# Kernel tuning notes

Hardware: AMD Instinct MI355X
Metric: run time of the kernel (lower is better)

## Reference

```python
import jax, jax.numpy as jnp
import numpy as np

N_P, E_P = 50000, 400000
N_L, E_L = 50000, 400000
B = 256  # number of graphs per side
NEG_GAT = 0.2   # GATv2 leaky-relu slope
NEG_FC = 0.01   # nn.LeakyReLU default slope


def _gatv2(x, ei, Wl, Wr, att, b, H, C):
    """GATv2Conv (concat heads, add_self_loops=True). Wl/Wr: [in, H*C], att: [H, C], b: [H*C]."""
    N = x.shape[0]
    sl = jnp.arange(N)
    src = jnp.concatenate([ei[0], sl])
    dst = jnp.concatenate([ei[1], sl])
    xl = (x @ Wl).reshape(N, H, C)   # source transform (messages)
    xr = (x @ Wr).reshape(N, H, C)   # target transform
    e = jax.nn.leaky_relu(xl[src] + xr[dst], NEG_GAT)          # [E+N, H, C]
    logits = jnp.einsum('ehc,hc->eh', e, att)                   # [E+N, H]
    m = jax.ops.segment_max(logits, dst, num_segments=N)        # segment softmax
    a = jnp.exp(logits - m[dst])
    alpha = a / jax.ops.segment_sum(a, dst, num_segments=N)[dst]
    out = jax.ops.segment_sum(xl[src] * alpha[..., None], dst, num_segments=N)
    return out.reshape(N, H * C) + b


def _mean_pool(x, batch, nb):
    s = jax.ops.segment_sum(x, batch, num_segments=nb)
    c = jax.ops.segment_sum(jnp.ones((x.shape[0],), x.dtype), batch, num_segments=nb)
    return s / jnp.maximum(c, 1.0)[:, None]


def setup_inputs() -> dict:
    key = jax.random.key(0)
    ks = jax.random.split(key, 48)
    i = [0]
    def nrm(shape, fan_in):
        k = ks[i[0]]; i[0] += 1
        return jax.random.normal(k, shape, jnp.float32) / np.sqrt(fan_in)
    inp = {}
    inp['protein_x'] = jax.random.normal(ks[40], (N_P, 10), jnp.float32)
    inp['ligand_x'] = jax.random.normal(ks[41], (N_L, 5), jnp.float32)
    inp['protein_edge_index'] = jax.random.randint(ks[42], (2, E_P), 0, N_P)
    inp['ligand_edge_index'] = jax.random.randint(ks[43], (2, E_L), 0, N_L)
    inp['protein_batch'] = (jnp.arange(N_P) * B) // N_P  # sorted graph ids, all segments nonempty
    inp['ligand_batch'] = (jnp.arange(N_L) * B) // N_L
    # GATv2 params: layer1 heads=2 out=128, layer2 heads=1 out=256
    inp['p1_Wl'] = nrm((10, 256), 10); inp['p1_Wr'] = nrm((10, 256), 10)
    inp['p1_att'] = nrm((2, 128), 128); inp['p1_b'] = jnp.zeros((256,), jnp.float32)
    inp['p2_Wl'] = nrm((256, 256), 256); inp['p2_Wr'] = nrm((256, 256), 256)
    inp['p2_att'] = nrm((1, 256), 256); inp['p2_b'] = jnp.zeros((256,), jnp.float32)
    inp['l1_Wl'] = nrm((5, 256), 5); inp['l1_Wr'] = nrm((5, 256), 5)
    inp['l1_att'] = nrm((2, 128), 128); inp['l1_b'] = jnp.zeros((256,), jnp.float32)
    inp['l2_Wl'] = nrm((256, 256), 256); inp['l2_Wr'] = nrm((256, 256), 256)
    inp['l2_att'] = nrm((1, 256), 256); inp['l2_b'] = jnp.zeros((256,), jnp.float32)
    # MultiheadAttention(256, 4) params ([in, out] convention)
    inp['Wq'] = nrm((256, 256), 256); inp['bq'] = jnp.zeros((256,), jnp.float32)
    inp['Wk'] = nrm((256, 256), 256); inp['bk'] = jnp.zeros((256,), jnp.float32)
    inp['Wv'] = nrm((256, 256), 256); inp['bv'] = jnp.zeros((256,), jnp.float32)
    inp['Wo'] = nrm((256, 256), 256); inp['bo'] = jnp.zeros((256,), jnp.float32)
    # fc head
    inp['fc1_w'] = nrm((512, 256), 512); inp['fc1_b'] = jnp.zeros((256,), jnp.float32)
    inp['ln_g'] = jnp.ones((256,), jnp.float32); inp['ln_b'] = jnp.zeros((256,), jnp.float32)
    inp['fc2_w'] = nrm((256, 1), 256); inp['fc2_b'] = jnp.zeros((1,), jnp.float32)
    return inp


def reference(protein_x, protein_edge_index, protein_batch,
              ligand_x, ligand_edge_index, ligand_batch,
              p1_Wl, p1_Wr, p1_att, p1_b, p2_Wl, p2_Wr, p2_att, p2_b,
              l1_Wl, l1_Wr, l1_att, l1_b, l2_Wl, l2_Wr, l2_att, l2_b,
              Wq, bq, Wk, bk, Wv, bv, Wo, bo,
              fc1_w, fc1_b, ln_g, ln_b, fc2_w, fc2_b):
    px = _gatv2(protein_x, protein_edge_index, p1_Wl, p1_Wr, p1_att, p1_b, 2, 128)
    px = _gatv2(px, protein_edge_index, p2_Wl, p2_Wr, p2_att, p2_b, 1, 256)
    px = _mean_pool(px, protein_batch, B)                        # [B, 256]
    lx = _gatv2(ligand_x, ligand_edge_index, l1_Wl, l1_Wr, l1_att, l1_b, 2, 128)
    lx = _gatv2(lx, ligand_edge_index, l2_Wl, l2_Wr, l2_att, l2_b, 1, 256)
    lx = _mean_pool(lx, ligand_batch, B)                         # [B, 256]
    # cross attention with q/k/v seq length 1
    D, H = 256, 4
    d = D // H
    qh = (px @ Wq + bq).reshape(B, H, d)
    kh = (lx @ Wk + bk).reshape(B, H, d)
    vh = (lx @ Wv + bv).reshape(B, H, d)
    scores = (qh * kh).sum(-1) / jnp.sqrt(jnp.float32(d))        # [B, H], 1 key
    w = jax.nn.softmax(scores[..., None], axis=-1)               # all ones (single key)
    attn = (w * vh).reshape(B, D) @ Wo + bo                      # [B, 256]
    comb = jnp.concatenate([px, attn], axis=1)                   # [B, 512]
    h = comb @ fc1_w + fc1_b
    mu = h.mean(-1, keepdims=True)
    var = h.var(-1, keepdims=True)
    h = (h - mu) / jnp.sqrt(var + 1e-5) * ln_g + ln_b
    h = jax.nn.leaky_relu(h, NEG_FC)
    return h @ fc2_w + fc2_b                                     # [B, 1]
```

## Files before the change

### kernel.cpp

```cpp
#include <hip/hip_runtime.h>
#include <math.h>

typedef unsigned short u16;
typedef __attribute__((ext_vector_type(8))) short bf16x8;
typedef __attribute__((ext_vector_type(4))) float f32x4;

__device__ inline u16 f2bf(float x) {
  unsigned int u = __float_as_uint(x);
  u += 0x7fffu + ((u >> 16) & 1u);
  return (u16)(u >> 16);
}
__device__ inline float bf2f(u16 h) {
  return __uint_as_float(((unsigned int)h) << 16);
}
__device__ inline float4 ld_bf4(const u16* p) {
  ushort4 v = *(const ushort4*)p;
  return make_float4(bf2f(v.x), bf2f(v.y), bf2f(v.z), bf2f(v.w));
}

__global__ void k_setup(int* __restrict__ cnt, int nz,
                        const float* __restrict__ W2pl, const float* __restrict__ W2pr,
                        const float* __restrict__ W2ll, const float* __restrict__ W2lr,
                        u16* __restrict__ Whp, u16* __restrict__ Wlp,
                        u16* __restrict__ Whl, u16* __restrict__ Wll_o,
                        const float* __restrict__ xp, int Kp, int Np,
                        const float* __restrict__ xl_, int Kl, int Nl,
                        const float* __restrict__ W1pl, const float* __restrict__ W1pr,
                        const float* __restrict__ W1ll, const float* __restrict__ W1lr,
                        u16* __restrict__ xlh_p, u16* __restrict__ xrh_p,
                        u16* __restrict__ xlh_l, u16* __restrict__ xrh_l,
                        int linPer) {
  const int zb = (nz + 255) / 256;
  if ((int)blockIdx.x < zb) {
    int i = blockIdx.x * 256 + threadIdx.x;
    if (i < nz) cnt[i] = 0;
    return;
  }
  int wb = blockIdx.x - zb;
  if (wb < 1024) {
    int n = wb & 511;
    int side = wb >> 9;
    int col = n & 255;
    int k = threadIdx.x;
    const float* W = side == 0 ? (n < 256 ? W2pl : W2pr) : (n < 256 ? W2ll : W2lr);
    float w = W[k * 256 + col];
    u16* Wh = side ? Whl : Whp;
    u16* Wlo = side ? Wll_o : Wlp;
    u16 hb = f2bf(w);
    Wh[n * 256 + k] = hb;
    Wlo[n * 256 + k] = f2bf(w - bf2f(hb));
    return;
  }
  int wb2 = wb - 1024;
  const int side = wb2 / linPer;
  const float* x = side ? xl_ : xp;
  const int K = side ? Kl : Kp;
  const int N = side ? Nl : Np;
  const float* Wl = side ? W1ll : W1pl;
  const float* Wr = side ? W1lr : W1pr;
  u16* xlh = side ? xlh_l : xlh_p;
  u16* xrh = side ? xrh_l : xrh_p;
  int base = (wb2 - side * linPer) * 8;
  if (base >= N) return;
  int j = threadIdx.x;
  __shared__ float xs[16][8];
  int tot = 8 * K;
  for (int i = j; i < tot; i += 256) {
    int r = i / K, k = i - r * K;
    if (base + r < N) xs[k][r] = x[(size_t)(base + r) * K + k];
  }
  __syncthreads();
  float al[8] = {}, ar[8] = {};
  for (int k = 0; k < K; ++k) {
    float wl = Wl[k * 256 + j];
    float wr = Wr[k * 256 + j];
#pragma unroll
    for (int r = 0; r < 8; ++r) {
      al[r] = fmaf(xs[k][r], wl, al[r]);
      ar[r] = fmaf(xs[k][r], wr, ar[r]);
    }
  }
#pragma unroll
  for (int r = 0; r < 8; ++r) {
    int n = base + r;
    if (n < N) {
      xlh[(size_t)n * 256 + j] = f2bf(al[r]);
      xrh[(size_t)n * 256 + j] = f2bf(ar[r]);
    }
  }
}

__global__ void k_histb(const int* __restrict__ eip, int Ep, const int* __restrict__ eil,
                        int El, int* __restrict__ cntp, int* __restrict__ cntl) {
  int e = blockIdx.x * blockDim.x + threadIdx.x;
  if (e < Ep) atomicAdd(&cntp[eip[Ep + e]], 1);
  else if (e < Ep + El) { int e2 = e - Ep; atomicAdd(&cntl[eil[El + e2]], 1); }
}

__global__ void k_scan1b(const int* __restrict__ cntp, int Np, const int* __restrict__ cntl,
                         int Nl, int nbp, int* __restrict__ offsp, int* __restrict__ offsl,
                         int* __restrict__ curp, int* __restrict__ curl,
                         int* __restrict__ bsum) {
  __shared__ int s[256];
  int tid = threadIdx.x;
  int side = ((int)blockIdx.x >= nbp) ? 1 : 0;
  int blk = side ? (blockIdx.x - nbp) : blockIdx.x;
  const int* cnt = side ? cntl : cntp;
  int* offs = side ? offsl : offsp;
  int* cur = side ? curl : curp;
  int N = side ? Nl : Np;
  int i = blk * 256 + tid;
  int v = (i < N) ? cnt[i] : 0;
  if (i < N) cur[i] = 0;
  s[tid] = v;
  __syncthreads();
  for (int off = 1; off < 256; off <<= 1) {
    int t = 0;
    if (tid >= off) t = s[tid - off];
    __syncthreads();
    if (tid >= off) s[tid] += t;
    __syncthreads();
  }
  if (i < N) offs[i] = s[tid] - v;
  if (tid == 255) bsum[side * 256 + blk] = s[255];
}

__global__ void k_scan2b(int* __restrict__ bsum, int nbp, int nbl) {
  __shared__ int s[256];
  int side = blockIdx.x;
  int nb = side ? nbl : nbp;
  int* bs = bsum + side * 256;
  int tid = threadIdx.x;
  int v = (tid < nb) ? bs[tid] : 0;
  s[tid] = v;
  __syncthreads();
  for (int off = 1; off < 256; off <<= 1) {
    int t = 0;
    if (tid >= off) t = s[tid - off];
    __syncthreads();
    if (tid >= off) s[tid] += t;
    __syncthreads();
  }
  if (tid < nb) bs[tid] = s[tid] - v;
}

__global__ void k_fillb(const int* __restrict__ eip, int Ep, const int* __restrict__ eil,
                        int El, const int* __restrict__ offsp, const int* __restrict__ offsl,
                        const int* __restrict__ bsum,
                        int* __restrict__ curp, int* __restrict__ curl,
                        int* __restrict__ csrp, int* __restrict__ csrl) {
  int e = blockIdx.x * blockDim.x + threadIdx.x;
  if (e < Ep) {
    int d = eip[Ep + e];
    int pos = offsp[d] + bsum[d >> 8] + atomicAdd(&curp[d], 1);
    csrp[pos] = eip[e];
  } else if (e < Ep + El) {
    int e2 = e - Ep;
    int d = eil[El + e2];
    int pos = offsl[d] + bsum[256 + (d >> 8)] + atomicAdd(&curl[d], 1);
    csrl[pos] = eil[e2];
  }
}

__global__ void __launch_bounds__(256, 2) k_mm_dual_b(
    const u16* __restrict__ A_p, const u16* __restrict__ A_l,
    const u16* __restrict__ Bh_p, const u16* __restrict__ Bl_p,
    const u16* __restrict__ Bh_l, const u16* __restrict__ Bl_l,
    u16* __restrict__ XLh_p, u16* __restrict__ XRh_p,
    u16* __restrict__ XLh_l, u16* __restrict__ XRh_l, int Np, int Nl, int Rp, int Rtot) {
  __shared__ __align__(16) char smem[32768];
  char* sA = smem;
  char* sBh = smem + 8192;
  char* sBl = smem + 16384;
  const int gid = blockIdx.x;
  const int rblk = (gid >> 5) * 8 + (gid & 7);
  const int col = (gid >> 3) & 3;
  if (rblk >= Rtot) return;
  const int side = (rblk >= Rp) ? 1 : 0;
  const int rloc = side ? rblk - Rp : rblk;
  const u16* A = side ? A_l : A_p;
  const u16* Bhi = side ? Bh_l : Bh_p;
  const u16* Blo = side ? Bl_l : Bl_p;
  u16* XLh = side ? XLh_l : XLh_p;
  u16* XRh = side ? XRh_l : XRh_p;
  const int M = side ? Nl : Np;
  const int t = threadIdx.x;
  const int rowBase = rloc * 128;
  const int j0 = col * 128;
  const int srow = t >> 1;
  const int h = t & 1;
  int gr = rowBase + srow;
  if (gr >= M) gr = M - 1;
  const size_t gaBase = (size_t)gr * 256 + h * 16;
  const size_t gbBase = (size_t)(j0 + srow) * 256 + h * 16;
  const int rb = srow * 64;
  const int sw0 = (((h * 2) + (srow >> 1)) & 3) * 16;
  const int sw1 = (((h * 2 + 1) + (srow >> 1)) & 3) * 16;
  const int lane = t & 63;
  const int wid = t >> 6;
  const int wm = (wid & 1) * 64;
  const int wn = (wid >> 1) * 64;
  const int kq = lane >> 4;
  const int mr = lane & 15;
  int offA[4], offB[4];
#pragma unroll
  for (int i = 0; i < 4; ++i) {
    int m = wm + i * 16 + mr;
    offA[i] = m * 64 + ((kq + (m >> 1)) & 3) * 16;
    int n = wn + i * 16 + mr;
    offB[i] = n * 64 + ((kq + (n >> 1)) & 3) * 16;
  }
  f32x4 acc[4][4] = {};
  uint4 va0 = *(const uint4*)(A + gaBase);
  uint4 va1 = *(const uint4*)(A + gaBase + 8);
  uint4 vbh0 = *(const uint4*)(Bhi + gbBase);
  uint4 vbh1 = *(const uint4*)(Bhi + gbBase + 8);
  uint4 vbl0 = *(const uint4*)(Blo + gbBase);
  uint4 vbl1 = *(const uint4*)(Blo + gbBase + 8);
#pragma unroll
  for (int kt = 0; kt < 8; ++kt) {
    __syncthreads();
    *(uint4*)(sA + rb + sw0) = va0;
    *(uint4*)(sA + rb + sw1) = va1;
    *(uint4*)(sBh + rb + sw0) = vbh0;
    *(uint4*)(sBh + rb + sw1) = vbh1;
    *(uint4*)(sBl + rb + sw0) = vbl0;
    *(uint4*)(sBl + rb + sw1) = vbl1;
    __syncthreads();
    if (kt < 7) {
      const int k0 = (kt + 1) * 32;
      va0 = *(const uint4*)(A + gaBase + k0);
      va1 = *(const uint4*)(A + gaBase + k0 + 8);
      vbh0 = *(const uint4*)(Bhi + gbBase + k0);
      vbh1 = *(const uint4*)(Bhi + gbBase + k0 + 8);
      vbl0 = *(const uint4*)(Blo + gbBase + k0);
      vbl1 = *(const uint4*)(Blo + gbBase + k0 + 8);
    }
    bf16x8 a[4], bh[4], bl[4];
#pragma unroll
    for (int i = 0; i < 4; ++i) {
      a[i] = *(const bf16x8*)(sA + offA[i]);
      bh[i] = *(const bf16x8*)(sBh + offB[i]);
      bl[i] = *(const bf16x8*)(sBl + offB[i]);
    }
#pragma unroll
    for (int i = 0; i < 4; ++i)
#pragma unroll
      for (int j = 0; j < 4; ++j) {
        acc[i][j] = __builtin_amdgcn_mfma_f32_16x16x32_bf16(a[i], bh[j], acc[i][j], 0, 0, 0);
        acc[i][j] = __builtin_amdgcn_mfma_f32_16x16x32_bf16(a[i], bl[j], acc[i][j], 0, 0, 0);
      }
  }
  __syncthreads();
  u16* wtile = (u16*)(smem + wid * 8192);
#pragma unroll
  for (int i = 0; i < 4; ++i)
#pragma unroll
    for (int j = 0; j < 4; ++j)
#pragma unroll
      for (int r = 0; r < 4; ++r)
        wtile[(i * 16 + kq * 4 + r) * 64 + j * 16 + mr] = f2bf(acc[i][j][r]);
  u16* cbase = (col < 2) ? XLh : XRh;
  const int cb = (col < 2) ? j0 : j0 - 256;
  const int r8 = lane >> 3;
  const int c8 = lane & 7;
#pragma unroll
  for (int rr = 0; rr < 8; ++rr) {
    int lr = rr * 8 + r8;
    uint4 v = *(const uint4*)&wtile[lr * 64 + c8 * 8];
    int row = rowBase + wm + lr;
    if (row < M) *(uint4*)&cbase[(size_t)row * 256 + cb + wn + c8 * 8] = v;
  }
}

#define GAT_DOT(a, q)                                                          \
  {                                                                            \
    float t0 = a.x + rd.x, t1 = a.y + rd.y, t2 = a.z + rd.z, t3 = a.w + rd.w;  \
    q = fmaf(t3, wa6.w, fabsf(t3) * wa4.w);                                    \
    q = fmaf(fabsf(t2), wa4.z, fmaf(t2, wa6.z, q));                            \
    q = fmaf(fabsf(t1), wa4.y, fmaf(t1, wa6.y, q));                            \
    q = fmaf(fabsf(t0), wa4.x, fmaf(t0, wa6.x, q));                            \
  }

template <int H>
__global__ void k_gat_gather_b(
    const u16* __restrict__ xlh_p, const u16* __restrict__ xrh_p, u16* __restrict__ out_p,
    const u16* __restrict__ xlh_l, const u16* __restrict__ xrh_l, u16* __restrict__ out_l,
    const int* __restrict__ csr_p, const int* __restrict__ offs_p,
    const int* __restrict__ cnt_p,
    const int* __restrict__ csr_l, const int* __restrict__ offs_l,
    const int* __restrict__ cnt_l, const int* __restrict__ bsum,
    const float* __restrict__ att_p, const float* __restrict__ bias_p,
    const float* __restrict__ att_l, const float* __restrict__ bias_l,
    int Np, int Nl) {
  const int side = blockIdx.y;
  const u16* xlh = side ? xlh_l : xlh_p;
  const u16* xrh = side ? xrh_l : xrh_p;
  u16* out = side ? out_l : out_p;
  const int* csr = side ? csr_l : csr_p;
  const int* offs = side ? offs_l : offs_p;
  const int* cnt = side ? cnt_l : cnt_p;
  const float* att = side ? att_l : att_p;
  const float* bias = side ? bias_l : bias_p;
  const int N = side ? Nl : Np;
  int d = blockIdx.x * 4 + (threadIdx.x >> 6);
  if (d >= N) return;
  const int lo4 = (threadIdx.x & 63) * 4;
  const float4 rd = ld_bf4(&xrh[(size_t)d * 256 + lo4]);
  const float4 wa = *(const float4*)&att[lo4];
  const float4 wa6 = make_float4(0.6f * wa.x, 0.6f * wa.y, 0.6f * wa.z, 0.6f * wa.w);
  const float4 wa4 = make_float4(0.4f * wa.x, 0.4f * wa.y, 0.4f * wa.z, 0.4f * wa.w);
  const float4 xd = ld_bf4(&xlh[(size_t)d * 256 + lo4]);
  float base;
  GAT_DOT(xd, base)
#pragma unroll
  for (int off = 1; off <= (H == 2 ? 16 : 32); off <<= 1) base += __shfl_xor(base, off, 64);
  float l0 = 1.f, l1 = 0.f, l2 = 0.f, l3 = 0.f;
  float4 acc0 = xd;
  float4 acc1 = make_float4(0.f, 0.f, 0.f, 0.f);
  float4 acc2 = make_float4(0.f, 0.f, 0.f, 0.f);
  float4 acc3 = make_float4(0.f, 0.f, 0.f, 0.f);
  const int o0 = offs[d] + bsum[side * 256 + (d >> 8)];
  const int c = cnt[d];
  int j = 0;
  for (; j + 3 < c; j += 4) {
    int s0 = csr[o0 + j], s1 = csr[o0 + j + 1], s2 = csr[o0 + j + 2], s3 = csr[o0 + j + 3];
    float4 a0 = ld_bf4(&xlh[(size_t)s0 * 256 + lo4]);
    float4 a1 = ld_bf4(&xlh[(size_t)s1 * 256 + lo4]);
    float4 a2 = ld_bf4(&xlh[(size_t)s2 * 256 + lo4]);
    float4 a3 = ld_bf4(&xlh[(size_t)s3 * 256 + lo4]);
    float q0, q1, q2, q3;
    GAT_DOT(a0, q0)
    GAT_DOT(a1, q1)
    GAT_DOT(a2, q2)
    GAT_DOT(a3, q3)
#pragma unroll
    for (int off = 1; off <= (H == 2 ? 16 : 32); off <<= 1) {
      q0 += __shfl_xor(q0, off, 64);
      q1 += __shfl_xor(q1, off, 64);
      q2 += __shfl_xor(q2, off, 64);
      q3 += __shfl_xor(q3, off, 64);
    }
    float w0 = __expf(q0 - base), w1 = __expf(q1 - base);
    float w2 = __expf(q2 - base), w3 = __expf(q3 - base);
    l0 += w0; l1 += w1; l2 += w2; l3 += w3;
    acc0.x = fmaf(w0, a0.x, acc0.x); acc0.y = fmaf(w0, a0.y, acc0.y);
    acc0.z = fmaf(w0, a0.z, acc0.z); acc0.w = fmaf(w0, a0.w, acc0.w);
    acc1.x = fmaf(w1, a1.x, acc1.x); acc1.y = fmaf(w1, a1.y, acc1.y);
    acc1.z = fmaf(w1, a1.z, acc1.z); acc1.w = fmaf(w1, a1.w, acc1.w);
    acc2.x = fmaf(w2, a2.x, acc2.x); acc2.y = fmaf(w2, a2.y, acc2.y);
    acc2.z = fmaf(w2, a2.z, acc2.z); acc2.w = fmaf(w2, a2.w, acc2.w);
    acc3.x = fmaf(w3, a3.x, acc3.x); acc3.y = fmaf(w3, a3.y, acc3.y);
    acc3.z = fmaf(w3, a3.z, acc3.z); acc3.w = fmaf(w3, a3.w, acc3.w);
  }
  for (; j < c; ++j) {
    int s0 = csr[o0 + j];
    float4 a0 = ld_bf4(&xlh[(size_t)s0 * 256 + lo4]);
    float q0;
    GAT_DOT(a0, q0)
#pragma unroll
    for (int off = 1; off <= (H == 2 ? 16 : 32); off <<= 1) q0 += __shfl_xor(q0, off, 64);
    float w0 = __expf(q0 - base);
    l0 += w0;
    acc0.x = fmaf(w0, a0.x, acc0.x); acc0.y = fmaf(w0, a0.y, acc0.y);
    acc0.z = fmaf(w0, a0.z, acc0.z); acc0.w = fmaf(w0, a0.w, acc0.w);
  }
  float inv = 1.f / (l0 + l1 + l2 + l3);
  float ax = acc0.x + acc1.x + acc2.x + acc3.x;
  float ay = acc0.y + acc1.y + acc2.y + acc3.y;
  float az = acc0.z + acc1.z + acc2.z + acc3.z;
  float aw = acc0.w + acc1.w + acc2.w + acc3.w;
  const float4 b4 = *(const float4*)&bias[lo4];
  ushort4 hv;
  hv.x = f2bf(ax * inv + b4.x);
  hv.y = f2bf(ay * inv + b4.y);
  hv.z = f2bf(az * inv + b4.z);
  hv.w = f2bf(aw * inv + b4.w);
  *(ushort4*)&out[(size_t)d * 256 + lo4] = hv;
}

#define POOL_C 8
__global__ void k_pool_part(const u16* __restrict__ xp, const int* __restrict__ bp, int Np,
                            const u16* __restrict__ xl_, const int* __restrict__ bl_, int Nl,
                            float* __restrict__ PPpart, float* __restrict__ LPpart) {
  const int b = blockIdx.x;
  const int side = blockIdx.y;
  const int chunk = blockIdx.z;
  const u16* x = side ? xl_ : xp;
  const int* batch = side ? bl_ : bp;
  const int N = side ? Nl : Np;
  float* part = side ? LPpart : PPpart;
  int j = threadIdx.x;
  __shared__ int sss, sse;
  if (j == 0) {
    int lo = 0, hi = N;
    while (lo < hi) { int mid = (lo + hi) >> 1; if (batch[mid] < b) lo = mid + 1; else hi = mid; }
    sss = lo;
    lo = 0; hi = N;
    while (lo < hi) { int mid = (lo + hi) >> 1; if (batch[mid] < b + 1) lo = mid + 1; else hi = mid; }
    sse = lo;
  }
  __syncthreads();
  int len = sse - sss;
  int per = (len + POOL_C - 1) / POOL_C;
  int st = sss + chunk * per;
  int en = st + per;
  if (en > sse) en = sse;
  float acc = 0.f;
  for (int n = st; n < en; ++n) acc += bf2f(x[(size_t)n * 256 + j]);
  part[((size_t)chunk * 256 + b) * 256 + j] = acc;
}

__global__ void k_head(const float* __restrict__ PPpart, const float* __restrict__ LPpart,
                       const int* __restrict__ bp, int Np,
                       const int* __restrict__ bl_, int Nl,
                       const float* __restrict__ Wv, const float* __restrict__ bv,
                       const float* __restrict__ Wo, const float* __restrict__ bo,
                       const float* __restrict__ fc1w, const float* __restrict__ fc1b,
                       const float* __restrict__ lng, const float* __restrict__ lnb,
                       const float* __restrict__ fc2w, const float* __restrict__ fc2b,
                       float* __restrict__ out) {
  int b = blockIdx.x;
  int j = threadIdx.x;
  __shared__ float lxs[256];
  __shared__ float vbuf[256];
  __shared__ float comb[512];
  __shared__ float r1[256], r2[256];
  __shared__ float smu, srs;
  __shared__ int seg[4];
  if (j < 2) {
    const int* batch = j ? bl_ : bp;
    int N = j ? Nl : Np;
    int lo = 0, hi = N;
    while (lo < hi) { int mid = (lo + hi) >> 1; if (batch[mid] < b) lo = mid + 1; else hi = mid; }
    seg[j * 2] = lo;
    lo = 0; hi = N;
    while (lo < hi) { int mid = (lo + hi) >> 1; if (batch[mid] < b + 1) lo = mid + 1; else hi = mid; }
    seg[j * 2 + 1] = lo;
  }
  __syncthreads();
  {
    float accp = 0.f, accl = 0.f;
#pragma unroll
    for (int c = 0; c < POOL_C; ++c) {
      accp += PPpart[((size_t)c * 256 + b) * 256 + j];
      accl += LPpart[((size_t)c * 256 + b) * 256 + j];
    }
    comb[j] = accp / fmaxf((float)(seg[1] - seg[0]), 1.f);
    lxs[j] = accl / fmaxf((float)(seg[3] - seg[2]), 1.f);
  }
  __syncthreads();
  {
    float v0 = 0.f, v1 = 0.f, v2 = 0.f, v3 = 0.f;
    for (int k = 0; k < 256; k += 4) {
      v0 = fmaf(lxs[k], Wv[k * 256 + j], v0);
      v1 = fmaf(lxs[k + 1], Wv[(k + 1) * 256 + j], v1);
      v2 = fmaf(lxs[k + 2], Wv[(k + 2) * 256 + j], v2);
      v3 = fmaf(lxs[k + 3], Wv[(k + 3) * 256 + j], v3);
    }
    vbuf[j] = bv[j] + ((v0 + v1) + (v2 + v3));
  }
  __syncthreads();
  {
    float a0 = 0.f, a1 = 0.f, a2 = 0.f, a3 = 0.f;
    for (int k = 0; k < 256; k += 4) {
      a0 = fmaf(vbuf[k], Wo[k * 256 + j], a0);
      a1 = fmaf(vbuf[k + 1], Wo[(k + 1) * 256 + j], a1);
      a2 = fmaf(vbuf[k + 2], Wo[(k + 2) * 256 + j], a2);
      a3 = fmaf(vbuf[k + 3], Wo[(k + 3) * 256 + j], a3);
    }
    comb[256 + j] = bo[j] + ((a0 + a1) + (a2 + a3));
  }
  __syncthreads();
  float h;
  {
    float h0 = 0.f, h1 = 0.f, h2 = 0.f, h3 = 0.f;
    for (int k = 0; k < 512; k += 4) {
      h0 = fmaf(comb[k], fc1w[k * 256 + j], h0);
      h1 = fmaf(comb[k + 1], fc1w[(k + 1) * 256 + j], h1);
      h2 = fmaf(comb[k + 2], fc1w[(k + 2) * 256 + j], h2);
      h3 = fmaf(comb[k + 3], fc1w[(k + 3) * 256 + j], h3);
    }
    h = fc1b[j] + ((h0 + h1) + (h2 + h3));
  }
  r1[j] = h;
  r2[j] = h * h;
  __syncthreads();
  for (int off = 128; off > 0; off >>= 1) {
    if (j < off) { r1[j] += r1[j + off]; r2[j] += r2[j + off]; }
    __syncthreads();
  }
  if (j == 0) {
    float mu = r1[0] / 256.f;
    float var = r2[0] / 256.f - mu * mu;
    smu = mu;
    srs = 1.f / sqrtf(var + 1e-5f);
  }
  __syncthreads();
  float hn = (h - smu) * srs * lng[j] + lnb[j];
  hn = hn > 0.f ? hn : 0.01f * hn;
  r1[j] = hn * fc2w[j];
  __syncthreads();
  for (int off = 128; off > 0; off >>= 1) {
    if (j < off) r1[j] += r1[j + off];
    __syncthreads();
  }
  if (j == 0) out[b] = r1[0] + fc2b[0];
}

extern "C" void kernel_launch(void* const* d_in, const int* in_sizes, int n_in,
                              void* d_out, int out_size, void* d_ws, size_t ws_size,
                              hipStream_t stream) {
  const float* px = (const float*)d_in[0];
  const float* lx = (const float*)d_in[1];
  const int* pei = (const int*)d_in[2];
  const int* lei = (const int*)d_in[3];
  const int* pb = (const int*)d_in[4];
  const int* lb = (const int*)d_in[5];
  const float* p1_Wl = (const float*)d_in[6];
  const float* p1_Wr = (const float*)d_in[7];
  const float* p1_att = (const float*)d_in[8];
  const float* p1_b = (const float*)d_in[9];
  const float* p2_Wl = (const float*)d_in[10];
  const float* p2_Wr = (const float*)d_in[11];
  const float* p2_att = (const float*)d_in[12];
  const float* p2_b = (const float*)d_in[13];
  const float* l1_Wl = (const float*)d_in[14];
  const float* l1_Wr = (const float*)d_in[15];
  const float* l1_att = (const float*)d_in[16];
  const float* l1_b = (const float*)d_in[17];
  const float* l2_Wl = (const float*)d_in[18];
  const float* l2_Wr = (const float*)d_in[19];
  const float* l2_att = (const float*)d_in[20];
  const float* l2_b = (const float*)d_in[21];
  const float* Wv = (const float*)d_in[26];
  const float* bv = (const float*)d_in[27];
  const float* Wo = (const float*)d_in[28];
  const float* bo = (const float*)d_in[29];
  const float* fc1w = (const float*)d_in[30];
  const float* fc1b = (const float*)d_in[31];
  const float* lng = (const float*)d_in[32];
  const float* lnb = (const float*)d_in[33];
  const float* fc2w = (const float*)d_in[34];
  const float* fc2b = (const float*)d_in[35];

  const int NPn = in_sizes[4];
  const int NLn = in_sizes[5];
  const int EPe = in_sizes[2] / 2;
  const int ELe = in_sizes[3] / 2;
  const int KP = in_sizes[0] / NPn;
  const int KL = in_sizes[1] / NLn;

  const int Nmax = NPn > NLn ? NPn : NLn;
  const int Emax = EPe > ELe ? EPe : ELe;
  size_t NF = (size_t)Nmax * 256;

  u16* XLh_p = (u16*)d_ws;
  u16* XRh_p = XLh_p + NF;
  u16* Ah_p = XRh_p + NF;
  u16* XLh_l = Ah_p + NF;
  u16* XRh_l = XLh_l + NF;
  u16* Ah_l = XRh_l + NF;
  u16* Wth = Ah_l + NF;
  u16* Wtl = Wth + 2 * 512 * 256;
  float* PPpart = (float*)(Wtl + 2 * 512 * 256);
  float* LPpart = PPpart + (size_t)POOL_C * 256 * 256;
  int* cnt = (int*)(LPpart + (size_t)POOL_C * 256 * 256);
  int* cur = cnt + 2 * (size_t)Nmax;
  int* offs = cur + 2 * (size_t)Nmax;
  int* bsum = offs + 2 * (size_t)Nmax;
  int* csr = bsum + 512;
  int* cnt_l = cnt + Nmax;
  int* cur_l = cur + Nmax;
  int* offs_l = offs + Nmax;
  int* csr_l = csr + Emax;

  const int nbp = (NPn + 255) / 256;
  const int nbl = (NLn + 255) / 256;
  const int nz = 2 * Nmax;
  const int zb = (nz + 255) / 256;
  const int linPer = (Nmax + 7) / 8;

  k_setup<<<zb + 1024 + 2 * linPer, 256, 0, stream>>>(
      cnt, nz, p2_Wl, p2_Wr, l2_Wl, l2_Wr,
      Wth, Wtl, Wth + 512 * 256, Wtl + 512 * 256,
      px, KP, NPn, lx, KL, NLn, p1_Wl, p1_Wr, l1_Wl, l1_Wr,
      XLh_p, XRh_p, XLh_l, XRh_l, linPer);
  k_histb<<<(EPe + ELe + 255) / 256, 256, 0, stream>>>(pei, EPe, lei, ELe, cnt, cnt_l);
  k_scan1b<<<nbp + nbl, 256, 0, stream>>>(cnt, NPn, cnt_l, NLn, nbp, offs, offs_l,
                                          cur, cur_l, bsum);
  k_scan2b<<<2, 256, 0, stream>>>(bsum, nbp, nbl);
  k_fillb<<<(EPe + ELe + 255) / 256, 256, 0, stream>>>(pei, EPe, lei, ELe, offs, offs_l,
                                                       bsum, cur, cur_l, csr, csr_l);
  k_gat_gather_b<2><<<dim3((Nmax + 3) / 4, 2), 256, 0, stream>>>(
      XLh_p, XRh_p, Ah_p, XLh_l, XRh_l, Ah_l,
      csr, offs, cnt, csr_l, offs_l, cnt_l, bsum,
      p1_att, p1_b, l1_att, l1_b, NPn, NLn);
  {
    const int Rp = (NPn + 127) / 128;
    const int Rl = (NLn + 127) / 128;
    const int Rtot = Rp + Rl;
    k_mm_dual_b<<<32 * ((Rtot + 7) / 8), 256, 0, stream>>>(
        Ah_p, Ah_l, Wth, Wtl, Wth + 512 * 256, Wtl + 512 * 256,
        XLh_p, XRh_p, XLh_l, XRh_l, NPn, NLn, Rp, Rtot);
  }
  k_gat_gather_b<1><<<dim3((Nmax + 3) / 4, 2), 256, 0, stream>>>(
      XLh_p, XRh_p, Ah_p, XLh_l, XRh_l, Ah_l,
      csr, offs, cnt, csr_l, offs_l, cnt_l, bsum,
      p2_att, p2_b, l2_att, l2_b, NPn, NLn);
  k_pool_part<<<dim3(256, 2, POOL_C), 256, 0, stream>>>(Ah_p, pb, NPn, Ah_l, lb, NLn,
                                                        PPpart, LPpart);
  k_head<<<256, 256, 0, stream>>>(PPpart, LPpart, pb, NPn, lb, NLn,
                                  Wv, bv, Wo, bo, fc1w, fc1b, lng, lnb, fc2w, fc2b,
                                  (float*)d_out);
  (void)n_in; (void)out_size; (void)ws_size;
}
```

Baseline: 524.5 us.

## Fold Wv·Wo·fc1 weight chain into precomputed matrix and use exp2 in GAT

```diff
diff --git a/kernel.cpp b/kernel.cpp
--- a/kernel.cpp
+++ b/kernel.cpp
@@ -4,6 +4,8 @@
 typedef unsigned short u16;
 typedef __attribute__((ext_vector_type(8))) short bf16x8;
 typedef __attribute__((ext_vector_type(4))) float f32x4;
+
+#define LOG2E 1.4426950408889634f
 
 __device__ inline u16 f2bf(float x) {
   unsigned int u = __float_as_uint(x);
@@ -29,7 +31,11 @@
                         const float* __restrict__ W1ll, const float* __restrict__ W1lr,
                         u16* __restrict__ xlh_p, u16* __restrict__ xrh_p,
                         u16* __restrict__ xlh_l, u16* __restrict__ xrh_l,
-                        int linPer) {
+                        int linPer,
+                        const float* __restrict__ Wo, const float* __restrict__ fc1w_,
+                        float* __restrict__ Wof) {
+  __shared__ float xs[16][8];
+  __shared__ float sW[256];
   const int zb = (nz + 255) / 256;
   if ((int)blockIdx.x < zb) {
     int i = blockIdx.x * 256 + threadIdx.x;
@@ -52,6 +58,22 @@
     return;
   }
   int wb2 = wb - 1024;
+  if (wb2 >= 2 * linPer) {
+    int row = wb2 - 2 * linPer;
+    if (row >= 256) return;
+    int jj = threadIdx.x;
+    sW[jj] = Wo[row * 256 + jj];
+    __syncthreads();
+    float a0 = 0.f, a1 = 0.f, a2 = 0.f, a3 = 0.f;
+    for (int c = 0; c < 256; c += 4) {
+      a0 = fmaf(sW[c], fc1w_[(256 + c) * 256 + jj], a0);
+      a1 = fmaf(sW[c + 1], fc1w_[(256 + c + 1) * 256 + jj], a1);
+      a2 = fmaf(sW[c + 2], fc1w_[(256 + c + 2) * 256 + jj], a2);
+      a3 = fmaf(sW[c + 3], fc1w_[(256 + c + 3) * 256 + jj], a3);
+    }
+    Wof[row * 256 + jj] = (a0 + a1) + (a2 + a3);
+    return;
+  }
   const int side = wb2 / linPer;
   const float* x = side ? xl_ : xp;
   const int K = side ? Kl : Kp;
@@ -63,7 +85,6 @@
   int base = (wb2 - side * linPer) * 8;
   if (base >= N) return;
   int j = threadIdx.x;
-  __shared__ float xs[16][8];
   int tot = 8 * K;
   for (int i = j; i < tot; i += 256) {
     int r = i / K, k = i - r * K;
@@ -91,7 +112,35 @@
 }
 
 __global__ void k_histb(const int* __restrict__ eip, int Ep, const int* __restrict__ eil,
-                        int El, int* __restrict__ cntp, int* __restrict__ cntl) {
+                        int El, int* __restrict__ cntp, int* __restrict__ cntl,
+                        int histB,
+                        const float* __restrict__ Wv, const float* __restrict__ Wof,
+                        const float* __restrict__ fc1w_, const float* __restrict__ bv,
+                        const float* __restrict__ bo, const float* __restrict__ fc1b,
+                        float* __restrict__ W2, float* __restrict__ biasEff) {
+  __shared__ float sV[256];
+  if ((int)blockIdx.x >= histB) {
+    int g2 = blockIdx.x - histB;
+    int jj = threadIdx.x;
+    if (g2 < 256) {
+      sV[jj] = Wv[g2 * 256 + jj];
+      __syncthreads();
+      float a0 = 0.f, a1 = 0.f, a2 = 0.f, a3 = 0.f;
+      for (int m = 0; m < 256; m += 4) {
+        a0 = fmaf(sV[m], Wof[m * 256 + jj], a0);
+        a1 = fmaf(sV[m + 1], Wof[(m + 1) * 256 + jj], a1);
+        a2 = fmaf(sV[m + 2], Wof[(m + 2) * 256 + jj], a2);
+        a3 = fmaf(sV[m + 3], Wof[(m + 3) * 256 + jj], a3);
+      }
+      W2[g2 * 256 + jj] = (a0 + a1) + (a2 + a3);
+    } else {
+      float acc = fc1b[jj];
+      for (int k = 0; k < 256; ++k) acc = fmaf(bv[k], Wof[k * 256 + jj], acc);
+      for (int k = 0; k < 256; ++k) acc = fmaf(bo[k], fc1w_[(256 + k) * 256 + jj], acc);
+      biasEff[jj] = acc;
+    }
+    return;
+  }
   int e = blockIdx.x * blockDim.x + threadIdx.x;
   if (e < Ep) atomicAdd(&cntp[eip[Ep + e]], 1);
   else if (e < Ep + El) { int e2 = e - Ep; atomicAdd(&cntl[eil[El + e2]], 1); }
@@ -308,8 +357,10 @@
   const int lo4 = (threadIdx.x & 63) * 4;
   const float4 rd = ld_bf4(&xrh[(size_t)d * 256 + lo4]);
   const float4 wa = *(const float4*)&att[lo4];
-  const float4 wa6 = make_float4(0.6f * wa.x, 0.6f * wa.y, 0.6f * wa.z, 0.6f * wa.w);
-  const float4 wa4 = make_float4(0.4f * wa.x, 0.4f * wa.y, 0.4f * wa.z, 0.4f * wa.w);
+  const float4 wa6 = make_float4(0.6f * LOG2E * wa.x, 0.6f * LOG2E * wa.y,
+                                 0.6f * LOG2E * wa.z, 0.6f * LOG2E * wa.w);
+  const float4 wa4 = make_float4(0.4f * LOG2E * wa.x, 0.4f * LOG2E * wa.y,
+                                 0.4f * LOG2E * wa.z, 0.4f * LOG2E * wa.w);
   const float4 xd = ld_bf4(&xlh[(size_t)d * 256 + lo4]);
   float base;
   GAT_DOT(xd, base)
@@ -341,8 +392,8 @@
       q2 += __shfl_xor(q2, off, 64);
       q3 += __shfl_xor(q3, off, 64);
     }
-    float w0 = __expf(q0 - base), w1 = __expf(q1 - base);
-    float w2 = __expf(q2 - base), w3 = __expf(q3 - base);
+    float w0 = __builtin_amdgcn_exp2f(q0 - base), w1 = __builtin_amdgcn_exp2f(q1 - base);
+    float w2 = __builtin_amdgcn_exp2f(q2 - base), w3 = __builtin_amdgcn_exp2f(q3 - base);
     l0 += w0; l1 += w1; l2 += w2; l3 += w3;
     acc0.x = fmaf(w0, a0.x, acc0.x); acc0.y = fmaf(w0, a0.y, acc0.y);
     acc0.z = fmaf(w0, a0.z, acc0.z); acc0.w = fmaf(w0, a0.w, acc0.w);
@@ -360,7 +411,7 @@
     GAT_DOT(a0, q0)
 #pragma unroll
     for (int off = 1; off <= (H == 2 ? 16 : 32); off <<= 1) q0 += __shfl_xor(q0, off, 64);
-    float w0 = __expf(q0 - base);
+    float w0 = __builtin_amdgcn_exp2f(q0 - base);
     l0 += w0;
     acc0.x = fmaf(w0, a0.x, acc0.x); acc0.y = fmaf(w0, a0.y, acc0.y);
     acc0.z = fmaf(w0, a0.z, acc0.z); acc0.w = fmaf(w0, a0.w, acc0.w);
@@ -414,98 +465,84 @@
 __global__ void k_head(const float* __restrict__ PPpart, const float* __restrict__ LPpart,
                        const int* __restrict__ bp, int Np,
                        const int* __restrict__ bl_, int Nl,
-                       const float* __restrict__ Wv, const float* __restrict__ bv,
-                       const float* __restrict__ Wo, const float* __restrict__ bo,
-                       const float* __restrict__ fc1w, const float* __restrict__ fc1b,
+                       const float* __restrict__ fc1w, const float* __restrict__ W2,
+                       const float* __restrict__ biasEff,
                        const float* __restrict__ lng, const float* __restrict__ lnb,
                        const float* __restrict__ fc2w, const float* __restrict__ fc2b,
                        float* __restrict__ out) {
   int b = blockIdx.x;
-  int j = threadIdx.x;
-  __shared__ float lxs[256];
-  __shared__ float vbuf[256];
-  __shared__ float comb[512];
+  int t = threadIdx.x;
+  int j = t & 255;
+  __shared__ float xs0[256], xs1[256];
+  __shared__ float part[2][256];
   __shared__ float r1[256], r2[256];
   __shared__ float smu, srs;
   __shared__ int seg[4];
-  if (j < 2) {
-    const int* batch = j ? bl_ : bp;
-    int N = j ? Nl : Np;
+  if (t < 2) {
+    const int* batch = t ? bl_ : bp;
+    int N = t ? Nl : Np;
     int lo = 0, hi = N;
     while (lo < hi) { int mid = (lo + hi) >> 1; if (batch[mid] < b) lo = mid + 1; else hi = mid; }
-    seg[j * 2] = lo;
+    seg[t * 2] = lo;
     lo = 0; hi = N;
     while (lo < hi) { int mid = (lo + hi) >> 1; if (batch[mid] < b + 1) lo = mid + 1; else hi = mid; }
-    seg[j * 2 + 1] = lo;
+    seg[t * 2 + 1] = lo;
+  }
+  __syncthreads();
+  if (t < 256) {
+    float accp = 0.f;
+#pragma unroll
+    for (int c = 0; c < POOL_C; ++c) accp += PPpart[((size_t)c * 256 + b) * 256 + j];
+    xs0[j] = accp / fmaxf((float)(seg[1] - seg[0]), 1.f);
+  } else {
+    float accl = 0.f;
+#pragma unroll
+    for (int c = 0; c < POOL_C; ++c) accl += LPpart[((size_t)c * 256 + b) * 256 + j];
+    xs1[j] = accl / fmaxf((float)(seg[3] - seg[2]), 1.f);
   }
   __syncthreads();
   {
-    float accp = 0.f, accl = 0.f;
-#pragma unroll
-    for (int c = 0; c < POOL_C; ++c) {
-      accp += PPpart[((size_t)c * 256 + b) * 256 + j];
-      accl += LPpart[((size_t)c * 256 + b) * 256 + j];
-    }
-    comb[j] = accp / fmaxf((float)(seg[1] - seg[0]), 1.f);
-    lxs[j] = accl / fmaxf((float)(seg[3] - seg[2]), 1.f);
-  }
-  __syncthreads();
-  {
-    float v0 = 0.f, v1 = 0.f, v2 = 0.f, v3 = 0.f;
-    for (int k = 0; k < 256; k += 4) {
-      v0 = fmaf(lxs[k], Wv[k * 256 + j], v0);
-      v1 = fmaf(lxs[k + 1], Wv[(k + 1) * 256 + j], v1);
-      v2 = fmaf(lxs[k + 2], Wv[(k + 2) * 256 + j], v2);
-      v3 = fmaf(lxs[k + 3], Wv[(k + 3) * 256 + j], v3);
-    }
-    vbuf[j] = bv[j] + ((v0 + v1) + (v2 + v3));
-  }
-  __syncthreads();
-  {
+    const float* src = (t < 256) ? xs0 : xs1;
+    const float* W = (t < 256) ? fc1w : W2;
     float a0 = 0.f, a1 = 0.f, a2 = 0.f, a3 = 0.f;
     for (int k = 0; k < 256; k += 4) {
-      a0 = fmaf(vbuf[k], Wo[k * 256 + j], a0);
-      a1 = fmaf(vbuf[k + 1], Wo[(k + 1) * 256 + j], a1);
-      a2 = fmaf(vbuf[k + 2], Wo[(k + 2) * 256 + j], a2);
-      a3 = fmaf(vbuf[k + 3], Wo[(k + 3) * 256 + j], a3);
-    }
-    comb[256 + j] = bo[j] + ((a0 + a1) + (a2 + a3));
-  }
-  __syncthreads();
-  float h;
-  {
-    float h0 = 0.f, h1 = 0.f, h2 = 0.f, h3 = 0.f;
-    for (int k = 0; k < 512; k += 4) {
-      h0 = fmaf(comb[k], fc1w[k * 256 + j], h0);
-      h1 = fmaf(comb[k + 1], fc1w[(k + 1) * 256 + j], h1);
-      h2 = fmaf(comb[k + 2], fc1w[(k + 2) * 256 + j], h2);
-      h3 = fmaf(comb[k + 3], fc1w[(k + 3) * 256 + j], h3);
-    }
-    h = fc1b[j] + ((h0 + h1) + (h2 + h3));
-  }
-  r1[j] = h;
-  r2[j] = h * h;
+      a0 = fmaf(src[k], W[k * 256 + j], a0);
+      a1 = fmaf(src[k + 1], W[(k + 1) * 256 + j], a1);
+      a2 = fmaf(src[k + 2], W[(k + 2) * 256 + j], a2);
+      a3 = fmaf(src[k + 3], W[(k + 3) * 256 + j], a3);
+    }
+    part[t >> 8][j] = (a0 + a1) + (a2 + a3);
+  }
+  __syncthreads();
+  float h = 0.f;
+  if (t < 256) {
+    h = part[0][j] + part[1][j] + biasEff[j];
+    r1[j] = h;
+    r2[j] = h * h;
+  }
   __syncthreads();
   for (int off = 128; off > 0; off >>= 1) {
-    if (j < off) { r1[j] += r1[j + off]; r2[j] += r2[j + off]; }
-    __syncthreads();
-  }
-  if (j == 0) {
+    if (t < off) { r1[t] += r1[t + off]; r2[t] += r2[t + off]; }
+    __syncthreads();
+  }
+  if (t == 0) {
     float mu = r1[0] / 256.f;
     float var = r2[0] / 256.f - mu * mu;
     smu = mu;
     srs = 1.f / sqrtf(var + 1e-5f);
   }
   __syncthreads();
-  float hn = (h - smu) * srs * lng[j] + lnb[j];
-  hn = hn > 0.f ? hn : 0.01f * hn;
-  r1[j] = hn * fc2w[j];
+  if (t < 256) {
+    float hn = (h - smu) * srs * lng[j] + lnb[j];
+    hn = hn > 0.f ? hn : 0.01f * hn;
+    r1[j] = hn * fc2w[j];
+  }
   __syncthreads();
   for (int off = 128; off > 0; off >>= 1) {
-    if (j < off) r1[j] += r1[j + off];
-    __syncthreads();
-  }
-  if (j == 0) out[b] = r1[0] + fc2b[0];
+    if (t < off) r1[t] += r1[t + off];
+    __syncthreads();
+  }
+  if (t == 0) out[b] = r1[0] + fc2b[0];
 }
 
 extern "C" void kernel_launch(void* const* d_in, const int* in_sizes, int n_in,
@@ -574,19 +611,24 @@
   int* cur_l = cur + Nmax;
   int* offs_l = offs + Nmax;
   int* csr_l = csr + Emax;
+  float* Wof = (float*)(csr + 2 * (size_t)Emax);
+  float* W2f = Wof + 65536;
+  float* bEff = W2f + 65536;
 
   const int nbp = (NPn + 255) / 256;
   const int nbl = (NLn + 255) / 256;
   const int nz = 2 * Nmax;
   const int zb = (nz + 255) / 256;
   const int linPer = (Nmax + 7) / 8;
-
-  k_setup<<<zb + 1024 + 2 * linPer, 256, 0, stream>>>(
+  const int histB = (EPe + ELe + 255) / 256;
+
+  k_setup<<<zb + 1024 + 2 * linPer + 256, 256, 0, stream>>>(
       cnt, nz, p2_Wl, p2_Wr, l2_Wl, l2_Wr,
       Wth, Wtl, Wth + 512 * 256, Wtl + 512 * 256,
       px, KP, NPn, lx, KL, NLn, p1_Wl, p1_Wr, l1_Wl, l1_Wr,
-      XLh_p, XRh_p, XLh_l, XRh_l, linPer);
-  k_histb<<<(EPe + ELe + 255) / 256, 256, 0, stream>>>(pei, EPe, lei, ELe, cnt, cnt_l);
+      XLh_p, XRh_p, XLh_l, XRh_l, linPer, Wo, fc1w, Wof);
+  k_histb<<<histB + 257, 256, 0, stream>>>(pei, EPe, lei, ELe, cnt, cnt_l, histB,
+                                           Wv, Wof, fc1w, bv, bo, fc1b, W2f, bEff);
   k_scan1b<<<nbp + nbl, 256, 0, stream>>>(cnt, NPn, cnt_l, NLn, nbp, offs, offs_l,
                                           cur, cur_l, bsum);
   k_scan2b<<<2, 256, 0, stream>>>(bsum, nbp, nbl);
@@ -610,8 +652,8 @@
       p2_att, p2_b, l2_att, l2_b, NPn, NLn);
   k_pool_part<<<dim3(256, 2, POOL_C), 256, 0, stream>>>(Ah_p, pb, NPn, Ah_l, lb, NLn,
                                                         PPpart, LPpart);
-  k_head<<<256, 256, 0, stream>>>(PPpart, LPpart, pb, NPn, lb, NLn,
-                                  Wv, bv, Wo, bo, fc1w, fc1b, lng, lnb, fc2w, fc2b,
+  k_head<<<256, 512, 0, stream>>>(PPpart, LPpart, pb, NPn, lb, NLn,
+                                  fc1w, W2f, bEff, lng, lnb, fc2w, fc2b,
                                   (float*)d_out);
   (void)n_in; (void)out_size; (void)ws_size;
 }
```

Result: no change. 518.5 us (-1.1%).
